# Kernel optimization log

Hardware: AMD Instinct MI355X
Metric: run time of the kernel (lower is better)

## Reference

```python
import jax, jax.numpy as jnp
import numpy as np

N_NODES = 50000
N_EDGES = 800000
IN_FEATS = 128
SAGE_HID = 512
H_FEATS = 128
MLP_HID = 32
N_PARTS = 8


def setup_inputs() -> dict:
    key = jax.random.key(0)
    ks = jax.random.split(key, 16)
    s = 0.05
    return {
        "features": jax.random.normal(ks[0], (N_NODES, IN_FEATS), jnp.float32),
        "src": jax.random.randint(ks[1], (N_EDGES,), 0, N_NODES),
        "dst": jax.random.randint(ks[2], (N_EDGES,), 0, N_NODES),
        # SAGEConv layer 1 (in_feats -> 512): fc_self has bias, fc_neigh no bias
        "W1_self": jax.random.normal(ks[3], (IN_FEATS, SAGE_HID), jnp.float32) * s,
        "W1_neigh": jax.random.normal(ks[4], (IN_FEATS, SAGE_HID), jnp.float32) * s,
        "b1": jnp.zeros((SAGE_HID,), jnp.float32),
        # SAGEConv layer 2 (512 -> h_feats)
        "W2_self": jax.random.normal(ks[5], (SAGE_HID, H_FEATS), jnp.float32) * s,
        "W2_neigh": jax.random.normal(ks[6], (SAGE_HID, H_FEATS), jnp.float32) * s,
        "b2": jnp.zeros((H_FEATS,), jnp.float32),
        # Partitioning MLP
        "Wp1": jax.random.normal(ks[7], (H_FEATS, MLP_HID), jnp.float32) * s,
        "bp1": jnp.zeros((MLP_HID,), jnp.float32),
        "Wp2": jax.random.normal(ks[8], (MLP_HID, N_PARTS), jnp.float32) * s,
        "bp2": jnp.zeros((N_PARTS,), jnp.float32),
    }


def _sage_mean(x, src, dst, deg_inv, W_self, W_neigh, b):
    # gather source-node features per edge, sum by destination, divide by in-degree
    agg = jax.ops.segment_sum(jnp.take(x, src, axis=0), dst, num_segments=N_NODES)
    agg = agg * deg_inv[:, None]
    return x @ W_self + agg @ W_neigh + b


def reference(features, src, dst, W1_self, W1_neigh, b1, W2_self, W2_neigh, b2,
              Wp1, bp1, Wp2, bp2):
    deg = jax.ops.segment_sum(jnp.ones_like(dst, dtype=features.dtype), dst,
                              num_segments=N_NODES)
    deg_inv = 1.0 / jnp.maximum(deg, 1.0)
    h = jax.nn.relu(_sage_mean(features, src, dst, deg_inv, W1_self, W1_neigh, b1))
    h = jax.nn.relu(_sage_mean(h, src, dst, deg_inv, W2_self, W2_neigh, b2))
    x = jax.nn.relu(h @ Wp1 + bp1)
    logits = x @ Wp2 + bp2
    return jax.nn.softmax(logits, axis=1)
```

## Files before the change

### kernel.cpp

```cpp
#include <hip/hip_runtime.h>
#include <hip/hip_bf16.h>

#define N_NODES 50000
#define N_EDGES 800000

typedef short  short8  __attribute__((ext_vector_type(8)));
typedef float  floatx4 __attribute__((ext_vector_type(4)));

__device__ __forceinline__ short f2bf(float f) {
    union { __hip_bfloat16 h; short s; } u;
    u.h = __float2bfloat16(f);
    return u.s;
}
__device__ __forceinline__ float2 upk(unsigned v) {
    union { float f; unsigned u; } a, b;
    a.u = v << 16; b.u = v & 0xffff0000u;
    return make_float2(a.f, b.f);
}
__device__ __forceinline__ unsigned packbf(float lo, float hi) {
    return ((unsigned)(unsigned short)f2bf(hi) << 16) | (unsigned short)f2bf(lo);
}

__device__ __forceinline__ void gld_lds16(const short* g, short* l) {
    __builtin_amdgcn_global_load_lds(
        (const __attribute__((address_space(1))) int*)g,
        (__attribute__((address_space(3))) int*)l, 16, 0, 0);
}

__global__ void k_deg(const int* __restrict__ dst, int* __restrict__ deg) {
    int e = blockIdx.x * 256 + threadIdx.x;
    if (e < N_EDGES) atomicAdd(&deg[dst[e]], 1);
}

__global__ __launch_bounds__(1024) void k_scan1(const int* __restrict__ deg,
                                                int* __restrict__ bsum,
                                                float* __restrict__ dinv) {
    __shared__ int ws[16];
    int b = blockIdx.x, t = threadIdx.x, i = b * 1024 + t;
    int lane = t & 63, wid = t >> 6;
    int v = (i < N_NODES) ? deg[i] : 0;
    if (i < N_NODES) dinv[i] = 1.0f / fmaxf((float)v, 1.0f);
    int x = v;
    #pragma unroll
    for (int off = 1; off < 64; off <<= 1) x += __shfl_xor(x, off, 64);
    if (lane == 0) ws[wid] = x;
    __syncthreads();
    if (t == 0) {
        int s = 0;
        #pragma unroll
        for (int k = 0; k < 16; ++k) s += ws[k];
        bsum[b] = s;
    }
}

__global__ void k_scan2(const int* __restrict__ bsum, int* __restrict__ boff) {
    int lane = threadIdx.x;
    int v = (lane < 49) ? bsum[lane] : 0;
    int x = v;
    #pragma unroll
    for (int off = 1; off < 64; off <<= 1) {
        int y = __shfl_up(x, off, 64);
        if (lane >= off) x += y;
    }
    if (lane < 49) boff[lane] = x - v;
}

__global__ __launch_bounds__(1024) void k_scan3(const int* __restrict__ deg,
                                                const int* __restrict__ boff,
                                                int* __restrict__ rowptr,
                                                int* __restrict__ cursor) {
    __shared__ int ws[16];
    int b = blockIdx.x, t = threadIdx.x, i = b * 1024 + t;
    int lane = t & 63, wid = t >> 6;
    int v = (i < N_NODES) ? deg[i] : 0;
    int x = v;
    #pragma unroll
    for (int off = 1; off < 64; off <<= 1) {
        int y = __shfl_up(x, off, 64);
        if (lane >= off) x += y;
    }
    if (lane == 63) ws[wid] = x;
    __syncthreads();
    if (wid == 0) {
        int s = (lane < 16) ? ws[lane] : 0;
        #pragma unroll
        for (int off = 1; off < 16; off <<= 1) {
            int y = __shfl_up(s, off, 64);
            if (lane >= off) s += y;
        }
        if (lane < 16) ws[lane] = s;
    }
    __syncthreads();
    int waveOff = (wid == 0) ? 0 : ws[wid - 1];
    int incl = x + waveOff + boff[b];
    if (i < N_NODES) { rowptr[i + 1] = incl; cursor[i] = incl - v; }
    if (b == 0 && t == 0) rowptr[0] = 0;
}

__global__ void k_fill(const int* __restrict__ src, const int* __restrict__ dst,
                       int* __restrict__ cursor, int* __restrict__ col) {
    int e = blockIdx.x * 256 + threadIdx.x;
    if (e < N_EDGES) {
        int d = dst[e];
        int p = atomicAdd(&cursor[d], 1);
        col[p] = src[e];
    }
}

__global__ void k_cvt(const float* __restrict__ feat,
                      const float* __restrict__ W1s, const float* __restrict__ W1n,
                      const float* __restrict__ W2s, const float* __restrict__ W2n,
                      short* __restrict__ Abf, short* __restrict__ W1T,
                      short* __restrict__ W2T) {
    int bb = blockIdx.x, t = threadIdx.x;
    if (bb < 6250) {
        int idx = bb * 256 + t;
        if (idx >= N_NODES * 32) return;
        int n = idx >> 5, c = (idx & 31) * 4;
        float4 v = *(const float4*)(feat + (size_t)n * 128 + c);
        *(short4*)(Abf + (size_t)n * 256 + c) =
            make_short4(f2bf(v.x), f2bf(v.y), f2bf(v.z), f2bf(v.w));
    } else {
        int idx = (bb - 6250) * 256 + t;
        if (idx < 512 * 256) {
            int n = idx >> 8, k = idx & 255;
            float v = (k < 128) ? W1s[(size_t)k * 512 + n]
                                : W1n[(size_t)(k - 128) * 512 + n];
            W1T[idx] = f2bf(v);
        } else {
            int j = idx - 512 * 256;
            int n = j >> 9, k = j & 511;
            float v = (n < 128) ? W2s[(size_t)k * 128 + n]
                                : W2n[(size_t)k * 128 + (n - 128)];
            W2T[j] = f2bf(v);
        }
    }
}

template<int STRIDE>
__device__ __forceinline__ float2 wave_gather(
    const unsigned* __restrict__ U, const int* __restrict__ col,
    int s, int e, int lane) {
    float ax = 0.f, ay = 0.f;
    for (int base = s; base < e; base += 64) {
        int cnt = e - base; if (cnt > 64) cnt = 64;
        int myc = (base + lane < e) ? col[base + lane] : 0;
        int j = 0;
        for (; j + 16 <= cnt; j += 16) {
            unsigned v[16];
            #pragma unroll
            for (int u = 0; u < 16; ++u) {
                int c = __builtin_amdgcn_readlane(myc, j + u);
                v[u] = U[(size_t)c * STRIDE + lane];
            }
            #pragma unroll
            for (int u = 0; u < 16; ++u) {
                float2 f = upk(v[u]); ax += f.x; ay += f.y;
            }
        }
        for (; j + 8 <= cnt; j += 8) {
            unsigned v[8];
            #pragma unroll
            for (int u = 0; u < 8; ++u) {
                int c = __builtin_amdgcn_readlane(myc, j + u);
                v[u] = U[(size_t)c * STRIDE + lane];
            }
            #pragma unroll
            for (int u = 0; u < 8; ++u) {
                float2 f = upk(v[u]); ax += f.x; ay += f.y;
            }
        }
        if (j < cnt) {
            unsigned v[8];
            int m = cnt - j;
            #pragma unroll
            for (int u = 0; u < 8; ++u) {
                if (u < m) {
                    int c = __builtin_amdgcn_readlane(myc, j + u);
                    v[u] = U[(size_t)c * STRIDE + lane];
                }
            }
            #pragma unroll
            for (int u = 0; u < 8; ++u) {
                if (u < m) { float2 f = upk(v[u]); ax += f.x; ay += f.y; }
            }
        }
    }
    return make_float2(ax, ay);
}

__global__ __launch_bounds__(256) void k_agg(
    const unsigned* __restrict__ Au, const int* __restrict__ rowptr,
    const int* __restrict__ col, const float* __restrict__ dinv,
    unsigned* __restrict__ Aw) {
    int t = threadIdx.x, lane = t & 63, w = t >> 6;
    int n = blockIdx.x * 4 + w;
    int s = rowptr[n], e = rowptr[n + 1];
    float2 a = wave_gather<128>(Au, col, s, e, lane);
    float dv = dinv[n];
    Aw[(size_t)n * 128 + 64 + lane] = packbf(a.x * dv, a.y * dv);
}

__global__ __launch_bounds__(256) void k_aggmlp(
    const unsigned* __restrict__ Yu, const int* __restrict__ rowptr,
    const int* __restrict__ col, const float* __restrict__ dinv,
    const float* __restrict__ z, const float* __restrict__ b2,
    const float* __restrict__ Wp1, const float* __restrict__ bp1,
    const float* __restrict__ Wp2, const float* __restrict__ bp2,
    float* __restrict__ out) {
    __shared__ float h2sh[4][128];
    __shared__ float xsh[4][32];
    int t = threadIdx.x, lane = t & 63, w = t >> 6;
    int n = blockIdx.x * 4 + w;
    int s = rowptr[n], e = rowptr[n + 1];
    float2 a = wave_gather<64>(Yu, col, s, e, lane);
    float dv = dinv[n];
    float2 zv = *(const float2*)(z + (size_t)n * 128 + 2 * lane);
    float2 bb = *(const float2*)(b2 + 2 * lane);
    h2sh[w][2 * lane]     = fmaxf(zv.x + a.x * dv + bb.x, 0.f);
    h2sh[w][2 * lane + 1] = fmaxf(zv.y + a.y * dv + bb.y, 0.f);
    int j = lane & 31, half = lane >> 5;
    float p = 0.f;
    #pragma unroll
    for (int k2 = 0; k2 < 64; ++k2) {
        int k = half * 64 + k2;
        p += h2sh[w][k] * Wp1[k * 32 + j];
    }
    p += __shfl_xor(p, 32, 64);
    if (half == 0) xsh[w][j] = fmaxf(p + bp1[j], 0.f);
    if (lane < 8) {
        float lg = bp2[lane];
        #pragma unroll
        for (int jj = 0; jj < 32; ++jj)
            lg += xsh[w][jj] * Wp2[jj * 8 + lane];
        float mx = lg;
        mx = fmaxf(mx, __shfl_xor(mx, 1, 64));
        mx = fmaxf(mx, __shfl_xor(mx, 2, 64));
        mx = fmaxf(mx, __shfl_xor(mx, 4, 64));
        float ev = expf(lg - mx);
        float sm = ev;
        sm += __shfl_xor(sm, 1, 64);
        sm += __shfl_xor(sm, 2, 64);
        sm += __shfl_xor(sm, 4, 64);
        out[(size_t)n * 8 + lane] = ev / sm;
    }
}

template<int K, int N, bool EPI1>
__global__ __launch_bounds__(256) void k_gemm_mfma(
    const short* __restrict__ A, const short* __restrict__ BT,
    const float* __restrict__ bias, short* __restrict__ Obf,
    float* __restrict__ Of0) {
    __shared__ short smem[2 * 128 * 32];
    short* sA = smem;
    short* sB = smem + 128 * 32;
    short* sOut = smem;
    const int t = threadIdx.x;
    const int lane = t & 63;
    const int w = t >> 6;
    const int mBase = blockIdx.x * 128;
    const int nBase = blockIdx.y * 128;
    const int mOff = (w & 1) * 64;
    const int nOff = (w >> 1) * 64;

    floatx4 zero4 = {0.f, 0.f, 0.f, 0.f};
    floatx4 acc[4][4];
    #pragma unroll
    for (int i = 0; i < 4; ++i)
        #pragma unroll
        for (int j = 0; j < 4; ++j) acc[i][j] = zero4;

    const int rL = lane >> 2;
    const int cg = (((lane & 3) ^ ((lane >> 3) & 3))) * 8;
    const int rA = w * 32 + rL;
    const long gA0 = (long)min(mBase + rA,      N_NODES - 1) * K + cg;
    const long gA1 = (long)min(mBase + rA + 16, N_NODES - 1) * K + cg;
    const long gB0 = (long)(nBase + rA)      * K + cg;
    const long gB1 = (long)(nBase + rA + 16) * K + cg;
    short* lA0 = sA + (w * 32) * 32;
    short* lA1 = sA + (w * 32 + 16) * 32;
    short* lB0 = sB + (w * 32) * 32;
    short* lB1 = sB + (w * 32 + 16) * 32;

    const int fr = lane & 15;
    const int csel = (((lane >> 4) ^ ((lane >> 1) & 3))) * 8;

    for (int kt = 0; kt < K / 32; ++kt) {
        const int k0 = kt * 32;
        __syncthreads();
        gld_lds16(A + gA0 + k0, lA0);
        gld_lds16(A + gA1 + k0, lA1);
        gld_lds16(BT + gB0 + k0, lB0);
        gld_lds16(BT + gB1 + k0, lB1);
        __syncthreads();
        short8 af[4], bf[4];
        #pragma unroll
        for (int i = 0; i < 4; ++i) {
            af[i] = *(const short8*)(sA + (mOff + i * 16 + fr) * 32 + csel);
            bf[i] = *(const short8*)(sB + (nOff + i * 16 + fr) * 32 + csel);
        }
        #pragma unroll
        for (int mi = 0; mi < 4; ++mi)
            #pragma unroll
            for (int ni = 0; ni < 4; ++ni)
                acc[mi][ni] = __builtin_amdgcn_mfma_f32_16x16x32_bf16(
                    af[mi], bf[ni], acc[mi][ni], 0, 0, 0);
    }

    const int cn = lane & 15;
    const int cm = (lane >> 4) * 4;

    if (!EPI1 && nBase < 128) {
        #pragma unroll
        for (int ni = 0; ni < 4; ++ni) {
            const int n = nOff + ni * 16 + cn;
            #pragma unroll
            for (int mi = 0; mi < 4; ++mi) {
                #pragma unroll
                for (int r = 0; r < 4; ++r) {
                    const int m = mBase + mOff + mi * 16 + cm + r;
                    if (m < N_NODES) Of0[(size_t)m * 128 + n] = acc[mi][ni][r];
                }
            }
        }
        return;
    }

    float bv[4];
    #pragma unroll
    for (int ni = 0; ni < 4; ++ni)
        bv[ni] = EPI1 ? bias[nBase + nOff + ni * 16 + cn] : 0.f;
    const int myh = mOff >> 6;
    const int ldc = EPI1 ? N : 128;
    const int cbase = EPI1 ? nBase : 0;
    for (int h = 0; h < 2; ++h) {
        __syncthreads();
        if (myh == h) {
            #pragma unroll
            for (int mi = 0; mi < 4; ++mi)
                #pragma unroll
                for (int ni = 0; ni < 4; ++ni)
                    #pragma unroll
                    for (int r = 0; r < 4; ++r) {
                        int mrow = mi * 16 + cm + r;
                        int nloc = nOff + ni * 16 + cn;
                        float v = acc[mi][ni][r];
                        if (EPI1) v = fmaxf(v + bv[ni], 0.f);
                        sOut[mrow * 128 + nloc] = f2bf(v);
                    }
        }
        __syncthreads();
        int r0 = t >> 2, c0 = (t & 3) * 32;
        int m = mBase + h * 64 + r0;
        if (m < N_NODES) {
            const short* sp = sOut + r0 * 128 + c0;
            short* gp = Obf + (size_t)m * ldc + cbase + c0;
            #pragma unroll
            for (int q = 0; q < 4; ++q)
                *(short8*)(gp + q * 8) = *(const short8*)(sp + q * 8);
        }
    }
}

extern "C" void kernel_launch(void* const* d_in, const int* in_sizes, int n_in,
                              void* d_out, int out_size, void* d_ws, size_t ws_size,
                              hipStream_t stream) {
    const float* feat   = (const float*)d_in[0];
    const int*   src    = (const int*)d_in[1];
    const int*   dst    = (const int*)d_in[2];
    const float* W1s    = (const float*)d_in[3];
    const float* W1n    = (const float*)d_in[4];
    const float* b1     = (const float*)d_in[5];
    const float* W2s    = (const float*)d_in[6];
    const float* W2n    = (const float*)d_in[7];
    const float* b2     = (const float*)d_in[8];
    const float* Wp1    = (const float*)d_in[9];
    const float* bp1    = (const float*)d_in[10];
    const float* Wp2    = (const float*)d_in[11];
    const float* bp2    = (const float*)d_in[12];
    float* out = (float*)d_out;

    char* w = (char*)d_ws;
    size_t off = 0;
    auto alloc = [&](size_t bytes) { char* p = w + off; off += (bytes + 255) & ~(size_t)255; return p; };
    int*   deg    = (int*)alloc(N_NODES * 4);
    int*   rowptr = (int*)alloc((N_NODES + 1) * 4);
    int*   cursor = (int*)alloc(N_NODES * 4);
    int*   col    = (int*)alloc(N_EDGES * 4);
    float* dinv   = (float*)alloc(N_NODES * 4);
    int*   bsum   = (int*)alloc(64 * 4);
    int*   boff   = (int*)alloc(64 * 4);
    short* Abf    = (short*)alloc((size_t)N_NODES * 256 * 2);
    short* W1T    = (short*)alloc((size_t)512 * 256 * 2);
    short* W2T    = (short*)alloc((size_t)256 * 512 * 2);
    short* h1bf   = (short*)alloc((size_t)N_NODES * 512 * 2);
    float* z      = (float*)alloc((size_t)N_NODES * 128 * 4);
    short* y1bf   = (short*)alloc((size_t)N_NODES * 128 * 2);

    hipMemsetAsync(deg, 0, N_NODES * 4, stream);
    k_deg<<<N_EDGES / 256, 256, 0, stream>>>(dst, deg);
    k_scan1<<<49, 1024, 0, stream>>>(deg, bsum, dinv);
    k_scan2<<<1, 64, 0, stream>>>(bsum, boff);
    k_scan3<<<49, 1024, 0, stream>>>(deg, boff, rowptr, cursor);
    k_fill<<<N_EDGES / 256, 256, 0, stream>>>(src, dst, cursor, col);
    k_cvt<<<7274, 256, 0, stream>>>(feat, W1s, W1n, W2s, W2n, Abf, W1T, W2T);
    k_agg<<<N_NODES / 4, 256, 0, stream>>>((const unsigned*)Abf, rowptr, col, dinv, (unsigned*)Abf);
    dim3 g1((N_NODES + 127) / 128, 4);
    k_gemm_mfma<256, 512, true><<<g1, 256, 0, stream>>>(Abf, W1T, b1, h1bf, nullptr);
    dim3 g2((N_NODES + 127) / 128, 2);
    k_gemm_mfma<512, 256, false><<<g2, 256, 0, stream>>>(h1bf, W2T, nullptr, y1bf, z);
    k_aggmlp<<<N_NODES / 4, 256, 0, stream>>>((const unsigned*)y1bf, rowptr, col, dinv, z, b2,
                                              Wp1, bp1, Wp2, bp2, out);
}
```

Measured before the change: 338.7 us.

## Gather four neighbor rows per wave with 16-byte vector loads

Restructures the per-node neighbor gather so each wave splits into four 16-lane groups. Each group handles a different edge and loads a full 128-byte bf16 row with uintx4 loads, and the partial sums are combined with cross-group shuffles. This cuts instruction count per edge and keeps more independent row loads in flight than the old one-dword-per-lane gather. In exchange it adds shuffle reductions, puts more pressure on accumulator registers, and leaves only 16 lanes active for the epilogue.

```diff
diff --git a/kernel.cpp b/kernel.cpp
--- a/kernel.cpp
+++ b/kernel.cpp
@@ -6,6 +6,7 @@
 
 typedef short  short8  __attribute__((ext_vector_type(8)));
 typedef float  floatx4 __attribute__((ext_vector_type(4)));
+typedef unsigned uintx4 __attribute__((ext_vector_type(4)));
 
 __device__ __forceinline__ short f2bf(float f) {
     union { __hip_bfloat16 h; short s; } u;
@@ -138,55 +139,70 @@
 }
 
 template<int STRIDE>
-__device__ __forceinline__ float2 wave_gather(
+__device__ __forceinline__ void wave_gather4(
     const unsigned* __restrict__ U, const int* __restrict__ col,
-    int s, int e, int lane) {
-    float ax = 0.f, ay = 0.f;
-    for (int base = s; base < e; base += 64) {
-        int cnt = e - base; if (cnt > 64) cnt = 64;
-        int myc = (base + lane < e) ? col[base + lane] : 0;
-        int j = 0;
-        for (; j + 16 <= cnt; j += 16) {
-            unsigned v[16];
-            #pragma unroll
-            for (int u = 0; u < 16; ++u) {
-                int c = __builtin_amdgcn_readlane(myc, j + u);
-                v[u] = U[(size_t)c * STRIDE + lane];
+    int s, int e, int lane, float ax[4], float ay[4]) {
+    const int g = lane >> 4;
+    const unsigned* Up = U + (lane & 15) * 4;
+    #pragma unroll
+    for (int q = 0; q < 4; ++q) { ax[q] = 0.f; ay[q] = 0.f; }
+    const int d = e - s;
+    const int nf = d >> 2;
+    int j = 0;
+    for (; j + 8 <= nf; j += 8) {
+        int cc[8];
+        #pragma unroll
+        for (int u = 0; u < 8; ++u) cc[u] = col[s + (j + u) * 4 + g];
+        uintx4 v[8];
+        #pragma unroll
+        for (int u = 0; u < 8; ++u)
+            v[u] = *(const uintx4*)(Up + (size_t)cc[u] * STRIDE);
+        #pragma unroll
+        for (int u = 0; u < 8; ++u)
+            #pragma unroll
+            for (int q = 0; q < 4; ++q) {
+                float2 f = upk(v[u][q]); ax[q] += f.x; ay[q] += f.y;
             }
-            #pragma unroll
-            for (int u = 0; u < 16; ++u) {
-                float2 f = upk(v[u]); ax += f.x; ay += f.y;
+    }
+    for (; j + 4 <= nf; j += 4) {
+        int cc[4];
+        #pragma unroll
+        for (int u = 0; u < 4; ++u) cc[u] = col[s + (j + u) * 4 + g];
+        uintx4 v[4];
+        #pragma unroll
+        for (int u = 0; u < 4; ++u)
+            v[u] = *(const uintx4*)(Up + (size_t)cc[u] * STRIDE);
+        #pragma unroll
+        for (int u = 0; u < 4; ++u)
+            #pragma unroll
+            for (int q = 0; q < 4; ++q) {
+                float2 f = upk(v[u][q]); ax[q] += f.x; ay[q] += f.y;
             }
-        }
-        for (; j + 8 <= cnt; j += 8) {
-            unsigned v[8];
-            #pragma unroll
-            for (int u = 0; u < 8; ++u) {
-                int c = __builtin_amdgcn_readlane(myc, j + u);
-                v[u] = U[(size_t)c * STRIDE + lane];
-            }
-            #pragma unroll
-            for (int u = 0; u < 8; ++u) {
-                float2 f = upk(v[u]); ax += f.x; ay += f.y;
-            }
-        }
-        if (j < cnt) {
-            unsigned v[8];
-            int m = cnt - j;
-            #pragma unroll
-            for (int u = 0; u < 8; ++u) {
-                if (u < m) {
-                    int c = __builtin_amdgcn_readlane(myc, j + u);
-                    v[u] = U[(size_t)c * STRIDE + lane];
-                }
-            }
-            #pragma unroll
-            for (int u = 0; u < 8; ++u) {
-                if (u < m) { float2 f = upk(v[u]); ax += f.x; ay += f.y; }
-            }
-        }
-    }
-    return make_float2(ax, ay);
+    }
+    for (; j < nf; ++j) {
+        int c = col[s + j * 4 + g];
+        uintx4 v = *(const uintx4*)(Up + (size_t)c * STRIDE);
+        #pragma unroll
+        for (int q = 0; q < 4; ++q) {
+            float2 f = upk(v[q]); ax[q] += f.x; ay[q] += f.y;
+        }
+    }
+    const int rem = d & 3;
+    if (rem && g < rem) {
+        int c = col[s + nf * 4 + g];
+        uintx4 v = *(const uintx4*)(Up + (size_t)c * STRIDE);
+        #pragma unroll
+        for (int q = 0; q < 4; ++q) {
+            float2 f = upk(v[q]); ax[q] += f.x; ay[q] += f.y;
+        }
+    }
+    #pragma unroll
+    for (int q = 0; q < 4; ++q) {
+        ax[q] += __shfl_xor(ax[q], 16, 64);
+        ax[q] += __shfl_xor(ax[q], 32, 64);
+        ay[q] += __shfl_xor(ay[q], 16, 64);
+        ay[q] += __shfl_xor(ay[q], 32, 64);
+    }
 }
 
 __global__ __launch_bounds__(256) void k_agg(
@@ -196,9 +212,15 @@
     int t = threadIdx.x, lane = t & 63, w = t >> 6;
     int n = blockIdx.x * 4 + w;
     int s = rowptr[n], e = rowptr[n + 1];
-    float2 a = wave_gather<128>(Au, col, s, e, lane);
-    float dv = dinv[n];
-    Aw[(size_t)n * 128 + 64 + lane] = packbf(a.x * dv, a.y * dv);
+    float ax[4], ay[4];
+    wave_gather4<128>(Au, col, s, e, lane, ax, ay);
+    if (lane < 16) {
+        float dv = dinv[n];
+        uintx4 o;
+        #pragma unroll
+        for (int q = 0; q < 4; ++q) o[q] = packbf(ax[q] * dv, ay[q] * dv);
+        *(uintx4*)(Aw + (size_t)n * 128 + 64 + lane * 4) = o;
+    }
 }
 
 __global__ __launch_bounds__(256) void k_aggmlp(
@@ -213,12 +235,25 @@
     int t = threadIdx.x, lane = t & 63, w = t >> 6;
     int n = blockIdx.x * 4 + w;
     int s = rowptr[n], e = rowptr[n + 1];
-    float2 a = wave_gather<64>(Yu, col, s, e, lane);
+    float ax[4], ay[4];
+    wave_gather4<64>(Yu, col, s, e, lane, ax, ay);
     float dv = dinv[n];
-    float2 zv = *(const float2*)(z + (size_t)n * 128 + 2 * lane);
-    float2 bb = *(const float2*)(b2 + 2 * lane);
-    h2sh[w][2 * lane]     = fmaxf(zv.x + a.x * dv + bb.x, 0.f);
-    h2sh[w][2 * lane + 1] = fmaxf(zv.y + a.y * dv + bb.y, 0.f);
+    if (lane < 16) {
+        const float* zp = z + (size_t)n * 128 + lane * 8;
+        float4 z0 = *(const float4*)(zp);
+        float4 z1 = *(const float4*)(zp + 4);
+        float4 b0 = *(const float4*)(b2 + lane * 8);
+        float4 b1v = *(const float4*)(b2 + lane * 8 + 4);
+        float* hp = &h2sh[w][lane * 8];
+        hp[0] = fmaxf(z0.x + ax[0] * dv + b0.x, 0.f);
+        hp[1] = fmaxf(z0.y + ay[0] * dv + b0.y, 0.f);
+        hp[2] = fmaxf(z0.z + ax[1] * dv + b0.z, 0.f);
+        hp[3] = fmaxf(z0.w + ay[1] * dv + b0.w, 0.f);
+        hp[4] = fmaxf(z1.x + ax[2] * dv + b1v.x, 0.f);
+        hp[5] = fmaxf(z1.y + ay[2] * dv + b1v.y, 0.f);
+        hp[6] = fmaxf(z1.z + ax[3] * dv + b1v.z, 0.f);
+        hp[7] = fmaxf(z1.w + ay[3] * dv + b1v.w, 0.f);
+    }
     int j = lane & 31, half = lane >> 5;
     float p = 0.f;
     #pragma unroll
```

New measurement: 361.0 us. 1.07x slower.
